# Kernel optimization log

Measured on AMD Instinct MI355X. Metric: run time of the kernel, lower is better.

## Reference

```python
import jax, jax.numpy as jnp
import numpy as np

N_BATCHES = 32
FEAT = 32
NUM_BESSEL = 8
HID = 8
DIST = 5.0
EPS = 1e-6


def setup_inputs() -> dict:
    N, F, B, NB, H = 50000, FEAT, NUM_BESSEL, N_BATCHES, HID
    key = jax.random.key(0)
    k = jax.random.split(key, 16)
    pos = jax.random.normal(k[0], (N, 3), jnp.float32) * 10.0
    batch = jnp.sort(jax.random.randint(k[1], (N,), 0, NB)).astype(jnp.int32)
    node_features = jax.random.normal(k[2], (N, F), jnp.float32)
    bessel_weights = jnp.arange(1, B + 1, dtype=jnp.float32) * jnp.pi

    def w(kk, shape, fan):
        return jax.random.normal(kk, shape, jnp.float32) / np.sqrt(fan).astype(np.float32)

    return dict(
        pos=pos, batch=batch, node_features=node_features,
        bessel_weights=bessel_weights,
        W_q_dummy=w(k[3], (F, F), F),
        Wk_gen1=w(k[4], (B, H), B), Wk_gen2=w(k[5], (H, F * F), H),
        Wv_gen1=w(k[6], (B, H), B), Wv_gen2=w(k[7], (H, F * F), H),
        W_q_graph=w(k[8], (F, F), F),
        Wkg_gen1=w(k[9], (B, H), B), Wkg_gen2=w(k[10], (H, F * F), H),
        Wvg_gen1=w(k[11], (B, H), B), Wvg_gen2=w(k[12], (H, F * F), H),
        W_dot=w(k[13], (F, F), F),
        init_dummy=jax.random.normal(k[14], (F,), jnp.float32),
    )


def _bessel(x, bw):
    # BesselBasisNoCutoff: sin(n*pi*x)/(x+eps), x: (N,) -> (N, B)
    return jnp.sin(bw * x[..., None]) / (x[..., None] + EPS)


def _gen_weights(edge_emb, W1, W2, F):
    # FullyConnectedNet([B, H, F*F], silu): (N,2,B) -> (N,2,F,F)
    h = jax.nn.silu(edge_emb @ W1)
    return (h @ W2).reshape(edge_emb.shape[0], 2, F, F)


def reference(pos, batch, node_features, bessel_weights,
              W_q_dummy, Wk_gen1, Wk_gen2, Wv_gen1, Wv_gen2,
              W_q_graph, Wkg_gen1, Wkg_gen2, Wvg_gen1, Wvg_gen2,
              W_dot, init_dummy):
    F = FEAT
    NB = N_BATCHES
    inv_sqrtF = 1.0 / np.sqrt(F).astype(np.float32)

    # ---- dummy edge features (Bessel basis on distance to top/bottom z surface) ----
    z = pos[:, 2]
    z_min = jax.ops.segment_min(z, batch, num_segments=NB, indices_are_sorted=True)
    z_max = jax.ops.segment_max(z, batch, num_segments=NB, indices_are_sorted=True)
    bottom_len = z - z_min[batch] + DIST          # (N,)
    top_len = z_max[batch] + DIST - z             # (N,)
    edge_emb = jnp.stack([_bessel(bottom_len, bessel_weights),
                          _bessel(top_len, bessel_weights)], axis=1)  # (N,2,B)
    # lmax=0 spherical harmonics, component normalization -> constant scalar 1

    # ---- dummy-node update: attention dummy(query) <- graph nodes (key/value) ----
    dummy_features = jnp.broadcast_to(init_dummy, (NB, 2, F))          # (NB,2,F)
    q_dummy = (dummy_features @ W_q_dummy) * inv_sqrtF                 # (NB,2,F)
    qn = q_dummy[batch]                                                # (N,2,F)

    Wk = _gen_weights(edge_emb, Wk_gen1, Wk_gen2, F)                   # (N,2,F,F)
    Wv = _gen_weights(edge_emb, Wv_gen1, Wv_gen2, F)
    k_d = jnp.einsum('nf,nsfg->nsg', node_features, Wk) * inv_sqrtF    # (N,2,F)
    v_d = jnp.einsum('nf,nsfg->nsg', node_features, Wv) * inv_sqrtF

    # dot: FullyConnectedTensorProduct(q, k -> 0e), scaled by 1/sqrt(scale_dim)
    scores = jnp.einsum('nsf,nsg,fg->ns', qn, k_d, W_dot) / F * inv_sqrtF  # (N,2)

    # per-batch softmax over graph nodes (segment softmax)
    smax = jax.ops.segment_max(scores, batch, num_segments=NB, indices_are_sorted=True)
    ex = jnp.exp(scores - smax[batch])
    denom = jax.ops.segment_sum(ex, batch, num_segments=NB, indices_are_sorted=True)
    attn = ex / denom[batch]                                           # (N,2)
    agg = jax.ops.segment_sum(attn[..., None] * v_d, batch,
                              num_segments=NB, indices_are_sorted=True)  # (NB,2,F)
    dummy_out = dummy_features + agg

    # ---- graph-node update: attention node(query) <- 2 dummy nodes (key/value) ----
    q_g = (node_features @ W_q_graph) * inv_sqrtF                      # (N,F)
    Wkg = _gen_weights(edge_emb, Wkg_gen1, Wkg_gen2, F)                # (N,2,F,F)
    Wvg = _gen_weights(edge_emb, Wvg_gen1, Wvg_gen2, F)
    d_per_node = dummy_out[batch]                                      # (N,2,F)
    k_g = jnp.einsum('nsf,nsfg->nsg', d_per_node, Wkg) * inv_sqrtF
    v_g = jnp.einsum('nsf,nsfg->nsg', d_per_node, Wvg) * inv_sqrtF
    scores_g = jnp.einsum('nf,nsg,fg->ns', q_g, k_g, W_dot) / F * inv_sqrtF  # (N,2)
    attn_g = jax.nn.softmax(scores_g, axis=1)
    node_out = node_features + jnp.einsum('ns,nsf->nf', attn_g, v_g)
    return node_out, dummy_out
```

## Files before the change

### kernel.cpp

```cpp
#include <hip/hip_runtime.h>

#define NBATCH 32
#define DIST 5.0f
#define EPSV 1e-6f
#define INV_SQRT_F 0.17677669529663687f
#define SC_STAGE2 1.72633492e-4f
#define SL1 7
#define SL2 7

__device__ __forceinline__ float silu_f(float v) { return __fdividef(v, 1.0f + __expf(-v)); }

__device__ __forceinline__ unsigned f2key(float f) {
  unsigned u = __float_as_uint(f);
  return (u & 0x80000000u) ? ~u : (u | 0x80000000u);
}
__device__ __forceinline__ float key2f(unsigned k) {
  return (k & 0x80000000u) ? __uint_as_float(k ^ 0x80000000u) : __uint_as_float(~k);
}

__device__ __forceinline__ int lower_bound_i(const int* __restrict__ batch, int N, int key) {
  int lo = 0, hi = N;
  while (lo < hi) { int m = (lo + hi) >> 1; if (batch[m] < key) lo = m + 1; else hi = m; }
  return lo;
}

extern "C" __global__ __launch_bounds__(256)
void stage1_kernel(const float* __restrict__ pos,
                   const int*   __restrict__ batch,
                   const float* __restrict__ xfeat,
                   const float* __restrict__ bw,
                   const float* __restrict__ Wqd,
                   const float* __restrict__ Wk1,
                   const float* __restrict__ Wk2,
                   const float* __restrict__ Wv1,
                   const float* __restrict__ Wdot,
                   const float* __restrict__ initd,
                   float* __restrict__ ws_Tp,
                   float* __restrict__ ws_denp,
                   float* __restrict__ ws_zf,
                   int N)
{
  const int b = blockIdx.x / SL1, jb = blockIdx.x % SL1;
  const int tid = threadIdx.x;

  __shared__ unsigned s_ru[256];
  __shared__ float s_red[256];
  __shared__ float s_bw[8];
  __shared__ float s_q[32], s_c[32];
  __shared__ float s_Wa[8][8], s_Wb[8][8];
  __shared__ float s_Mk[32][8];
  __shared__ float s_exh[256][17];
  __shared__ float s_xs[256][36];
  __shared__ float s_Tp[4][512];

  if (tid < 8) s_bw[tid] = bw[tid];
  if (tid < 64) { s_Wa[tid >> 3][tid & 7] = Wk1[tid]; s_Wb[tid >> 3][tid & 7] = Wv1[tid]; }
  if (tid < 32) {
    float a = 0.f;
    #pragma unroll
    for (int f = 0; f < 32; f++) a += initd[f] * Wqd[f * 32 + tid];
    s_q[tid] = a * INV_SQRT_F;
  }
  const int ss0 = lower_bound_i(batch, N, b);
  const int ss1 = lower_bound_i(batch, N, b + 1);
  __syncthreads();
  if (tid < 32) {
    float a = 0.f;
    #pragma unroll
    for (int f = 0; f < 32; f++) a += s_q[f] * Wdot[f * 32 + tid];
    s_c[tid] = a;
  }
  __syncthreads();
  {
    int f = tid >> 3, h = tid & 7;
    const float* w = &Wk2[h * 1024 + f * 32];
    float a = 0.f;
    #pragma unroll
    for (int g = 0; g < 32; g++) a += w[g] * s_c[g];
    s_Mk[f][h] = a * (1.0f / 1024.0f);
  }

  unsigned kmn = 0xFFFFFFFFu, kmx = 0u;
  for (int i = ss0 + tid; i < ss1; i += 256) {
    unsigned k = f2key(pos[3 * (size_t)i + 2]);
    kmn = min(kmn, k); kmx = max(kmx, k);
  }
  s_ru[tid] = kmn; __syncthreads();
  for (int off = 128; off > 0; off >>= 1) { if (tid < off) s_ru[tid] = min(s_ru[tid], s_ru[tid + off]); __syncthreads(); }
  const unsigned rmn = s_ru[0]; __syncthreads();
  s_ru[tid] = kmx; __syncthreads();
  for (int off = 128; off > 0; off >>= 1) { if (tid < off) s_ru[tid] = max(s_ru[tid], s_ru[tid + off]); __syncthreads(); }
  const unsigned rmx = s_ru[0];
  __syncthreads();
  const float zmin = key2f(rmn), zmax = key2f(rmx);

  const int cnt = ss1 - ss0;
  const int per = (cnt + SL1 - 1) / SL1;
  const int lo = ss0 + jb * per;
  const int hi = min(lo + per, ss1);

  float Treg[8] = {0,0,0,0,0,0,0,0};
  float d0 = 0.f, d1 = 0.f;
  const int group = tid >> 6, gt = tid & 63, osh = gt >> 2, ofg = gt & 3;

  for (int base = lo; base < hi; base += 256) {
    int i = base + tid;
    if (i < hi) {
      float z = pos[3 * (size_t)i + 2];
      float len0 = z - zmin + DIST, len1 = zmax + DIST - z;
      float xv[32];
      const float4* xp = (const float4*)&xfeat[(size_t)i * 32];
      float4* xso = (float4*)s_xs[tid];
      #pragma unroll
      for (int q = 0; q < 8; q++) {
        float4 t = xp[q];
        xso[q] = t;
        xv[4*q] = t.x; xv[4*q+1] = t.y; xv[4*q+2] = t.z; xv[4*q+3] = t.w;
      }
      float u[8] = {0,0,0,0,0,0,0,0};
      #pragma unroll
      for (int f = 0; f < 32; f++) {
        float xf = xv[f];
        #pragma unroll
        for (int h = 0; h < 8; h++) u[h] += xf * s_Mk[f][h];
      }
      #pragma unroll
      for (int s = 0; s < 2; s++) {
        float L = s ? len1 : len0;
        float inv = __fdividef(1.0f, L + EPSV);
        float ee[8];
        #pragma unroll
        for (int j = 0; j < 8; j++) ee[j] = __sinf(s_bw[j] * L) * inv;
        float sc = 0.f;
        #pragma unroll
        for (int h = 0; h < 8; h++) {
          float a = 0.f;
          #pragma unroll
          for (int j = 0; j < 8; j++) a += ee[j] * s_Wa[j][h];
          sc += silu_f(a) * u[h];
        }
        float ex = __expf(fminf(fmaxf(sc, -60.f), 60.f));
        if (s) d1 += ex; else d0 += ex;
        #pragma unroll
        for (int h = 0; h < 8; h++) {
          float v = 0.f;
          #pragma unroll
          for (int j = 0; j < 8; j++) v += ee[j] * s_Wb[j][h];
          s_exh[tid][8*s + h] = ex * silu_f(v);
        }
      }
    } else {
      #pragma unroll
      for (int h = 0; h < 16; h++) s_exh[tid][h] = 0.f;
      float4* xso = (float4*)s_xs[tid];
      float4 z4 = make_float4(0.f, 0.f, 0.f, 0.f);
      #pragma unroll
      for (int q = 0; q < 8; q++) xso[q] = z4;
    }
    __syncthreads();
    const int cb = group * 64;
    for (int c = cb; c < cb + 64; c++) {
      float eh = s_exh[c][osh];
      const float4* xr4 = (const float4*)&s_xs[c][ofg * 8];
      float4 xa = xr4[0], xb = xr4[1];
      Treg[0] += eh * xa.x; Treg[1] += eh * xa.y; Treg[2] += eh * xa.z; Treg[3] += eh * xa.w;
      Treg[4] += eh * xb.x; Treg[5] += eh * xb.y; Treg[6] += eh * xb.z; Treg[7] += eh * xb.w;
    }
    __syncthreads();
  }
  #pragma unroll
  for (int k = 0; k < 8; k++) s_Tp[group][osh * 32 + ofg * 8 + k] = Treg[k];
  __syncthreads();
  const int slot = b * SL1 + jb;
  for (int idx = tid; idx < 512; idx += 256)
    ws_Tp[slot * 512 + idx] = s_Tp[0][idx] + s_Tp[1][idx] + s_Tp[2][idx] + s_Tp[3][idx];
  s_red[tid] = d0; __syncthreads();
  for (int off = 128; off > 0; off >>= 1) { if (tid < off) s_red[tid] += s_red[tid + off]; __syncthreads(); }
  if (tid == 0) ws_denp[slot * 2 + 0] = s_red[0];
  __syncthreads();
  s_red[tid] = d1; __syncthreads();
  for (int off = 128; off > 0; off >>= 1) { if (tid < off) s_red[tid] += s_red[tid + off]; __syncthreads(); }
  if (tid == 0) ws_denp[slot * 2 + 1] = s_red[0];
  if (jb == 0 && tid == 0) { ws_zf[2*b] = zmin; ws_zf[2*b+1] = zmax; }
}

extern "C" __global__ __launch_bounds__(256)
void stage2_kernel(const float* __restrict__ pos,
                   const int*   __restrict__ batch,
                   const float* __restrict__ xfeat,
                   const float* __restrict__ bw,
                   const float* __restrict__ Wqg,  const float* __restrict__ Wdot,
                   const float* __restrict__ Wkg1, const float* __restrict__ Wkg2,
                   const float* __restrict__ Wvg1, const float* __restrict__ Wvg2,
                   const float* __restrict__ Wv2,  const float* __restrict__ initd,
                   const float* __restrict__ ws_Tp,
                   const float* __restrict__ ws_denp,
                   const float* __restrict__ ws_zf,
                   float* __restrict__ out_node, float* __restrict__ out_dummy,
                   int N)
{
  const int b = blockIdx.x / SL2, jb = blockIdx.x % SL2;
  const int tid = threadIdx.x;

  __shared__ float s_bw[8];
  __shared__ float s_Wa[8][8], s_Wb[8][8];
  __shared__ float s_T[512];
  __shared__ float s_den[2];
  __shared__ float s_dp[4][2][32];
  __shared__ float s_dm[2][32];
  __shared__ float s_WQD[32][32];
  __shared__ float s_Bkg[16][32];
  __shared__ float s_Bvg[16][32];
  __shared__ float s_G[32][16];

  if (tid < 8) s_bw[tid] = bw[tid];
  if (tid < 64) { s_Wa[tid >> 3][tid & 7] = Wkg1[tid]; s_Wb[tid >> 3][tid & 7] = Wvg1[tid]; }
  if (tid < 2) {
    float d = 0.f;
    #pragma unroll
    for (int j = 0; j < SL1; j++) d += ws_denp[(b * SL1 + j) * 2 + tid];
    s_den[tid] = d;
  }
  for (int idx = tid; idx < 512; idx += 256) {
    float a = 0.f;
    #pragma unroll
    for (int j = 0; j < SL1; j++) a += ws_Tp[(b * SL1 + j) * 512 + idx];
    s_T[idx] = a;
  }
  for (int idx = tid; idx < 1024; idx += 256) {
    int f = idx >> 5, g = idx & 31;
    float a = 0.f;
    #pragma unroll
    for (int k = 0; k < 32; k++) a += Wqg[f * 32 + k] * Wdot[k * 32 + g];
    s_WQD[f][g] = a;
  }
  const int ss0 = lower_bound_i(batch, N, b);
  const int ss1 = lower_bound_i(batch, N, b + 1);
  const float zmin = ws_zf[2*b], zmax = ws_zf[2*b+1];
  __syncthreads();

  {
    int g = tid & 31, s = (tid >> 5) & 1, fq = tid >> 6;
    float acc = 0.f;
    #pragma unroll
    for (int h = 0; h < 8; h++) {
      #pragma unroll
      for (int f8 = 0; f8 < 8; f8++) {
        int f = fq * 8 + f8;
        acc += s_T[(8 * s + h) * 32 + f] * Wv2[h * 1024 + f * 32 + g];
      }
    }
    s_dp[fq][s][g] = acc;
  }
  __syncthreads();
  if (tid < 64) {
    int s = tid >> 5, g = tid & 31;
    float acc = s_dp[0][s][g] + s_dp[1][s][g] + s_dp[2][s][g] + s_dp[3][s][g];
    float dn = s_den[s];
    float dv = initd[g] + (dn > 0.f ? acc * INV_SQRT_F * __fdividef(1.0f, dn) : 0.f);
    s_dm[s][g] = dv;
    if (jb == 0) out_dummy[b * 64 + tid] = dv;
  }
  __syncthreads();
  for (int idx = tid; idx < 512; idx += 256) {
    int sh = idx >> 5, g = idx & 31, s = sh >> 3, h = sh & 7;
    const float* wk = &Wkg2[h * 1024 + g];
    const float* wv = &Wvg2[h * 1024 + g];
    float a = 0.f, v = 0.f;
    #pragma unroll
    for (int f = 0; f < 32; f++) { float d = s_dm[s][f]; a += d * wk[f * 32]; v += d * wv[f * 32]; }
    s_Bkg[sh][g] = a;
    s_Bvg[sh][g] = v;
  }
  __syncthreads();
  for (int idx = tid; idx < 512; idx += 256) {
    int f = idx >> 4, sh = idx & 15;
    float a = 0.f;
    #pragma unroll
    for (int g = 0; g < 32; g++) a += s_WQD[f][g] * s_Bkg[sh][g];
    s_G[f][sh] = a * SC_STAGE2;
  }
  __syncthreads();

  const int cnt = ss1 - ss0;
  const int per = (cnt + SL2 - 1) / SL2;
  const int lo = ss0 + tid + jb * per;
  const int hi = min(ss0 + (jb + 1) * per, ss1);

  for (int i = lo; i < hi; i += 256) {
    float z = pos[3 * (size_t)i + 2];
    float len0 = z - zmin + DIST, len1 = zmax + DIST - z;
    float ee[16];
    #pragma unroll
    for (int s = 0; s < 2; s++) {
      float L = s ? len1 : len0;
      float inv = __fdividef(1.0f, L + EPSV);
      #pragma unroll
      for (int j = 0; j < 8; j++) ee[8*s + j] = __sinf(s_bw[j] * L) * inv;
    }
    float hkg[16], hvg[16];
    #pragma unroll
    for (int s = 0; s < 2; s++) {
      #pragma unroll
      for (int h = 0; h < 8; h++) {
        float a = 0.f, v = 0.f;
        #pragma unroll
        for (int j = 0; j < 8; j++) { a += ee[8*s + j] * s_Wa[j][h]; v += ee[8*s + j] * s_Wb[j][h]; }
        hkg[8*s + h] = silu_f(a); hvg[8*s + h] = silu_f(v);
      }
    }
    float xv[32];
    const float4* xp = (const float4*)&xfeat[(size_t)i * 32];
    #pragma unroll
    for (int q = 0; q < 8; q++) { float4 t = xp[q]; xv[4*q] = t.x; xv[4*q+1] = t.y; xv[4*q+2] = t.z; xv[4*q+3] = t.w; }
    float ev[16] = {0,0,0,0,0,0,0,0,0,0,0,0,0,0,0,0};
    #pragma unroll
    for (int f = 0; f < 32; f++) {
      float xf = xv[f];
      #pragma unroll
      for (int sh = 0; sh < 16; sh++) ev[sh] += xf * s_G[f][sh];
    }
    float sc0 = 0.f, sc1 = 0.f;
    #pragma unroll
    for (int h = 0; h < 8; h++) { sc0 += hkg[h] * ev[h]; sc1 += hkg[8 + h] * ev[8 + h]; }
    float m = fmaxf(sc0, sc1);
    float a0 = __expf(sc0 - m), a1 = __expf(sc1 - m);
    float invd = __fdividef(1.0f, a0 + a1);
    float w0 = a0 * invd * INV_SQRT_F, w1 = a1 * invd * INV_SQRT_F;
    float wv[16];
    #pragma unroll
    for (int sh = 0; sh < 16; sh++) wv[sh] = (sh < 8 ? w0 : w1) * hvg[sh];
    float ov[32];
    #pragma unroll
    for (int g = 0; g < 32; g++) ov[g] = xv[g];
    #pragma unroll
    for (int sh = 0; sh < 16; sh++) {
      float w = wv[sh];
      #pragma unroll
      for (int g = 0; g < 32; g++) ov[g] += w * s_Bvg[sh][g];
    }
    float4* op = (float4*)&out_node[(size_t)i * 32];
    #pragma unroll
    for (int q = 0; q < 8; q++) op[q] = make_float4(ov[4*q], ov[4*q+1], ov[4*q+2], ov[4*q+3]);
  }
}

extern "C" void kernel_launch(void* const* d_in, const int* in_sizes, int n_in,
                              void* d_out, int out_size, void* d_ws, size_t ws_size,
                              hipStream_t stream)
{
  const float* pos   = (const float*)d_in[0];
  const int*   batch = (const int*)d_in[1];
  const float* xf    = (const float*)d_in[2];
  const float* bw    = (const float*)d_in[3];
  const float* Wqd   = (const float*)d_in[4];
  const float* Wk1   = (const float*)d_in[5];
  const float* Wk2   = (const float*)d_in[6];
  const float* Wv1   = (const float*)d_in[7];
  const float* Wv2   = (const float*)d_in[8];
  const float* Wqg   = (const float*)d_in[9];
  const float* Wkg1  = (const float*)d_in[10];
  const float* Wkg2  = (const float*)d_in[11];
  const float* Wvg1  = (const float*)d_in[12];
  const float* Wvg2  = (const float*)d_in[13];
  const float* Wdot  = (const float*)d_in[14];
  const float* initd = (const float*)d_in[15];
  int N = in_sizes[1];

  float* out_node  = (float*)d_out;
  float* out_dummy = out_node + (size_t)N * 32;

  float* ws      = (float*)d_ws;
  float* ws_Tp   = ws;
  float* ws_denp = ws + 114688;
  float* ws_zf   = ws + 115200;

  stage1_kernel<<<NBATCH * SL1, 256, 0, stream>>>(pos, batch, xf, bw, Wqd, Wk1, Wk2, Wv1,
                                                  Wdot, initd, ws_Tp, ws_denp, ws_zf, N);

  stage2_kernel<<<NBATCH * SL2, 256, 0, stream>>>(pos, batch, xf, bw, Wqg, Wdot, Wkg1, Wkg2,
                                                  Wvg1, Wvg2, Wv2, initd, ws_Tp, ws_denp,
                                                  ws_zf, out_node, out_dummy, N);
}
```

Before: 46.56 us.

## Split batches into eight slices and overlap per-slice loads with z min/max scan

Result: faster. 40.99 us (-12.0%).

```diff
diff --git a/kernel.cpp b/kernel.cpp
--- a/kernel.cpp
+++ b/kernel.cpp
@@ -5,8 +5,8 @@
 #define EPSV 1e-6f
 #define INV_SQRT_F 0.17677669529663687f
 #define SC_STAGE2 1.72633492e-4f
-#define SL1 7
-#define SL2 7
+#define SL1 8
+#define SL2 8
 
 __device__ __forceinline__ float silu_f(float v) { return __fdividef(v, 1.0f + __expf(-v)); }
 
@@ -40,11 +40,10 @@
                    float* __restrict__ ws_zf,
                    int N)
 {
-  const int b = blockIdx.x / SL1, jb = blockIdx.x % SL1;
+  const int b = blockIdx.x >> 3, jb = blockIdx.x & 7;
   const int tid = threadIdx.x;
-
-  __shared__ unsigned s_ru[256];
-  __shared__ float s_red[256];
+  const int wid = tid >> 6, lane = tid & 63;
+
   __shared__ float s_bw[8];
   __shared__ float s_q[32], s_c[32];
   __shared__ float s_Wa[8][8], s_Wb[8][8];
@@ -52,6 +51,8 @@
   __shared__ float s_exh[256][17];
   __shared__ float s_xs[256][36];
   __shared__ float s_Tp[4][512];
+  __shared__ unsigned s_wmin[4], s_wmax[4];
+  __shared__ float s_wd0[4], s_wd1[4];
 
   if (tid < 8) s_bw[tid] = bw[tid];
   if (tid < 64) { s_Wa[tid >> 3][tid & 7] = Wk1[tid]; s_Wb[tid >> 3][tid & 7] = Wv1[tid]; }
@@ -79,31 +80,115 @@
     for (int g = 0; g < 32; g++) a += w[g] * s_c[g];
     s_Mk[f][h] = a * (1.0f / 1024.0f);
   }
-
-  unsigned kmn = 0xFFFFFFFFu, kmx = 0u;
-  for (int i = ss0 + tid; i < ss1; i += 256) {
-    unsigned k = f2key(pos[3 * (size_t)i + 2]);
-    kmn = min(kmn, k); kmx = max(kmx, k);
-  }
-  s_ru[tid] = kmn; __syncthreads();
-  for (int off = 128; off > 0; off >>= 1) { if (tid < off) s_ru[tid] = min(s_ru[tid], s_ru[tid + off]); __syncthreads(); }
-  const unsigned rmn = s_ru[0]; __syncthreads();
-  s_ru[tid] = kmx; __syncthreads();
-  for (int off = 128; off > 0; off >>= 1) { if (tid < off) s_ru[tid] = max(s_ru[tid], s_ru[tid + off]); __syncthreads(); }
-  const unsigned rmx = s_ru[0];
-  __syncthreads();
-  const float zmin = key2f(rmn), zmax = key2f(rmx);
+  __syncthreads();
 
   const int cnt = ss1 - ss0;
   const int per = (cnt + SL1 - 1) / SL1;
   const int lo = ss0 + jb * per;
   const int hi = min(lo + per, ss1);
 
+  const int i0 = lo + tid;
+  const bool act = i0 < hi;
+  float4 xr[8];
+  float z0 = 0.f;
+  if (act) {
+    const float4* xp = (const float4*)&xfeat[(size_t)i0 * 32];
+    #pragma unroll
+    for (int q = 0; q < 8; q++) xr[q] = xp[q];
+    z0 = pos[3 * (size_t)i0 + 2];
+  }
+  unsigned kmn = 0xFFFFFFFFu, kmx = 0u;
+  for (int base = ss0; base < ss1; base += 2048) {
+    float zz[8]; int iv[8];
+    #pragma unroll
+    for (int q = 0; q < 8; q++) {
+      int i = base + (q << 8) + tid;
+      iv[q] = (i < ss1);
+      zz[q] = iv[q] ? pos[3 * (size_t)i + 2] : 0.f;
+    }
+    #pragma unroll
+    for (int q = 0; q < 8; q++) if (iv[q]) {
+      unsigned k = f2key(zz[q]);
+      kmn = min(kmn, k); kmx = max(kmx, k);
+    }
+  }
+  float u[8] = {0,0,0,0,0,0,0,0};
+  if (act) {
+    float4* xso = (float4*)s_xs[tid];
+    #pragma unroll
+    for (int q = 0; q < 8; q++) {
+      xso[q] = xr[q];
+      float vx0 = xr[q].x, vx1 = xr[q].y, vx2 = xr[q].z, vx3 = xr[q].w;
+      #pragma unroll
+      for (int h = 0; h < 8; h++)
+        u[h] += vx0 * s_Mk[4*q][h] + vx1 * s_Mk[4*q+1][h] + vx2 * s_Mk[4*q+2][h] + vx3 * s_Mk[4*q+3][h];
+    }
+  } else {
+    float4* xso = (float4*)s_xs[tid];
+    float4 z4 = make_float4(0.f, 0.f, 0.f, 0.f);
+    #pragma unroll
+    for (int q = 0; q < 8; q++) xso[q] = z4;
+  }
+  #pragma unroll
+  for (int m = 32; m >= 1; m >>= 1) {
+    kmn = min(kmn, (unsigned)__shfl_xor((int)kmn, m));
+    kmx = max(kmx, (unsigned)__shfl_xor((int)kmx, m));
+  }
+  if (lane == 0) { s_wmin[wid] = kmn; s_wmax[wid] = kmx; }
+  __syncthreads();
+  const unsigned rmn = min(min(s_wmin[0], s_wmin[1]), min(s_wmin[2], s_wmin[3]));
+  const unsigned rmx = max(max(s_wmax[0], s_wmax[1]), max(s_wmax[2], s_wmax[3]));
+  const float zmin = key2f(rmn), zmax = key2f(rmx);
+
   float Treg[8] = {0,0,0,0,0,0,0,0};
   float d0 = 0.f, d1 = 0.f;
-  const int group = tid >> 6, gt = tid & 63, osh = gt >> 2, ofg = gt & 3;
-
-  for (int base = lo; base < hi; base += 256) {
+  const int osh = lane >> 2, ofg = lane & 3;
+
+  if (act) {
+    float len0 = z0 - zmin + DIST, len1 = zmax + DIST - z0;
+    #pragma unroll
+    for (int s = 0; s < 2; s++) {
+      float L = s ? len1 : len0;
+      float inv = __fdividef(1.0f, L + EPSV);
+      float ee[8];
+      #pragma unroll
+      for (int j = 0; j < 8; j++) ee[j] = __sinf(s_bw[j] * L) * inv;
+      float sc = 0.f;
+      #pragma unroll
+      for (int h = 0; h < 8; h++) {
+        float a = 0.f;
+        #pragma unroll
+        for (int j = 0; j < 8; j++) a += ee[j] * s_Wa[j][h];
+        sc += silu_f(a) * u[h];
+      }
+      float ex = __expf(fminf(fmaxf(sc, -60.f), 60.f));
+      if (s) d1 += ex; else d0 += ex;
+      #pragma unroll
+      for (int h = 0; h < 8; h++) {
+        float v = 0.f;
+        #pragma unroll
+        for (int j = 0; j < 8; j++) v += ee[j] * s_Wb[j][h];
+        s_exh[tid][8*s + h] = ex * silu_f(v);
+      }
+    }
+  } else {
+    #pragma unroll
+    for (int h = 0; h < 16; h++) s_exh[tid][h] = 0.f;
+  }
+  __syncthreads();
+  {
+    const int cb = wid * 64;
+    for (int c = cb; c < cb + 64; c++) {
+      float eh = s_exh[c][osh];
+      const float4* xr4 = (const float4*)&s_xs[c][ofg * 8];
+      float4 xa = xr4[0], xb = xr4[1];
+      Treg[0] += eh * xa.x; Treg[1] += eh * xa.y; Treg[2] += eh * xa.z; Treg[3] += eh * xa.w;
+      Treg[4] += eh * xb.x; Treg[5] += eh * xb.y; Treg[6] += eh * xb.z; Treg[7] += eh * xb.w;
+    }
+  }
+  __syncthreads();
+
+  for (int base = lo + 256; base < hi; base += 256) {
     int i = base + tid;
     if (i < hi) {
       float z = pos[3 * (size_t)i + 2];
@@ -117,12 +202,12 @@
         xso[q] = t;
         xv[4*q] = t.x; xv[4*q+1] = t.y; xv[4*q+2] = t.z; xv[4*q+3] = t.w;
       }
-      float u[8] = {0,0,0,0,0,0,0,0};
+      float uu[8] = {0,0,0,0,0,0,0,0};
       #pragma unroll
       for (int f = 0; f < 32; f++) {
         float xf = xv[f];
         #pragma unroll
-        for (int h = 0; h < 8; h++) u[h] += xf * s_Mk[f][h];
+        for (int h = 0; h < 8; h++) uu[h] += xf * s_Mk[f][h];
       }
       #pragma unroll
       for (int s = 0; s < 2; s++) {
@@ -137,7 +222,7 @@
           float a = 0.f;
           #pragma unroll
           for (int j = 0; j < 8; j++) a += ee[j] * s_Wa[j][h];
-          sc += silu_f(a) * u[h];
+          sc += silu_f(a) * uu[h];
         }
         float ex = __expf(fminf(fmaxf(sc, -60.f), 60.f));
         if (s) d1 += ex; else d0 += ex;
@@ -158,7 +243,7 @@
       for (int q = 0; q < 8; q++) xso[q] = z4;
     }
     __syncthreads();
-    const int cb = group * 64;
+    const int cb = wid * 64;
     for (int c = cb; c < cb + 64; c++) {
       float eh = s_exh[c][osh];
       const float4* xr4 = (const float4*)&s_xs[c][ofg * 8];
@@ -168,20 +253,21 @@
     }
     __syncthreads();
   }
+
   #pragma unroll
-  for (int k = 0; k < 8; k++) s_Tp[group][osh * 32 + ofg * 8 + k] = Treg[k];
+  for (int k = 0; k < 8; k++) s_Tp[wid][osh * 32 + ofg * 8 + k] = Treg[k];
+  #pragma unroll
+  for (int m = 32; m >= 1; m >>= 1) { d0 += __shfl_xor(d0, m); d1 += __shfl_xor(d1, m); }
+  if (lane == 0) { s_wd0[wid] = d0; s_wd1[wid] = d1; }
   __syncthreads();
   const int slot = b * SL1 + jb;
   for (int idx = tid; idx < 512; idx += 256)
     ws_Tp[slot * 512 + idx] = s_Tp[0][idx] + s_Tp[1][idx] + s_Tp[2][idx] + s_Tp[3][idx];
-  s_red[tid] = d0; __syncthreads();
-  for (int off = 128; off > 0; off >>= 1) { if (tid < off) s_red[tid] += s_red[tid + off]; __syncthreads(); }
-  if (tid == 0) ws_denp[slot * 2 + 0] = s_red[0];
-  __syncthreads();
-  s_red[tid] = d1; __syncthreads();
-  for (int off = 128; off > 0; off >>= 1) { if (tid < off) s_red[tid] += s_red[tid + off]; __syncthreads(); }
-  if (tid == 0) ws_denp[slot * 2 + 1] = s_red[0];
-  if (jb == 0 && tid == 0) { ws_zf[2*b] = zmin; ws_zf[2*b+1] = zmax; }
+  if (tid == 0) {
+    ws_denp[slot * 2 + 0] = s_wd0[0] + s_wd0[1] + s_wd0[2] + s_wd0[3];
+    ws_denp[slot * 2 + 1] = s_wd1[0] + s_wd1[1] + s_wd1[2] + s_wd1[3];
+    if (jb == 0) { ws_zf[2*b] = zmin; ws_zf[2*b+1] = zmax; }
+  }
 }
 
 extern "C" __global__ __launch_bounds__(256)
@@ -199,7 +285,7 @@
                    float* __restrict__ out_node, float* __restrict__ out_dummy,
                    int N)
 {
-  const int b = blockIdx.x / SL2, jb = blockIdx.x % SL2;
+  const int b = blockIdx.x >> 3, jb = blockIdx.x & 7;
   const int tid = threadIdx.x;
 
   __shared__ float s_bw[8];
@@ -237,6 +323,12 @@
   const int ss0 = lower_bound_i(batch, N, b);
   const int ss1 = lower_bound_i(batch, N, b + 1);
   const float zmin = ws_zf[2*b], zmax = ws_zf[2*b+1];
+  const int cnt = ss1 - ss0;
+  const int per = (cnt + SL2 - 1) / SL2;
+  const int lo = ss0 + jb * per;
+  const int hi = min(ss0 + (jb + 1) * per, ss1);
+  const int i0 = lo + tid;
+  const float z0 = (i0 < hi) ? pos[3 * (size_t)i0 + 2] : 0.f;
   __syncthreads();
 
   {
@@ -282,13 +374,8 @@
   }
   __syncthreads();
 
-  const int cnt = ss1 - ss0;
-  const int per = (cnt + SL2 - 1) / SL2;
-  const int lo = ss0 + tid + jb * per;
-  const int hi = min(ss0 + (jb + 1) * per, ss1);
-
-  for (int i = lo; i < hi; i += 256) {
-    float z = pos[3 * (size_t)i + 2];
+  for (int i = i0; i < hi; i += 256) {
+    float z = (i == i0) ? z0 : pos[3 * (size_t)i + 2];
     float len0 = z - zmin + DIST, len1 = zmax + DIST - z;
     float ee[16];
     #pragma unroll
@@ -327,15 +414,15 @@
     float a0 = __expf(sc0 - m), a1 = __expf(sc1 - m);
     float invd = __fdividef(1.0f, a0 + a1);
     float w0 = a0 * invd * INV_SQRT_F, w1 = a1 * invd * INV_SQRT_F;
-    float wv[16];
-    #pragma unroll
-    for (int sh = 0; sh < 16; sh++) wv[sh] = (sh < 8 ? w0 : w1) * hvg[sh];
+    float wvv[16];
+    #pragma unroll
+    for (int sh = 0; sh < 16; sh++) wvv[sh] = (sh < 8 ? w0 : w1) * hvg[sh];
     float ov[32];
     #pragma unroll
     for (int g = 0; g < 32; g++) ov[g] = xv[g];
     #pragma unroll
     for (int sh = 0; sh < 16; sh++) {
-      float w = wv[sh];
+      float w = wvv[sh];
       #pragma unroll
       for (int g = 0; g < 32; g++) ov[g] += w * s_Bvg[sh][g];
     }
@@ -372,8 +459,8 @@
 
   float* ws      = (float*)d_ws;
   float* ws_Tp   = ws;
-  float* ws_denp = ws + 114688;
-  float* ws_zf   = ws + 115200;
+  float* ws_denp = ws + 131072;
+  float* ws_zf   = ws + 131584;
 
   stage1_kernel<<<NBATCH * SL1, 256, 0, stream>>>(pos, batch, xf, bw, Wqd, Wk1, Wk2, Wv1,
                                                   Wdot, initd, ws_Tp, ws_denp, ws_zf, N);
```
